# Optimization experiments

Measured on AMD Instinct MI355X. Metric: run time of the kernel, lower is better.

## Reference

```python
import jax, jax.numpy as jnp
import numpy as np

N_NODES = 50000

def _sage_conv(x, src, dst, W_l, b_l, W_r):
    # PyG SAGEConv, aggr='mean': out = lin_l(mean_j x_j) + lin_r(x_i)
    msg = x[src]                                                 # [E, d] gather
    agg = jax.ops.segment_sum(msg, dst, num_segments=N_NODES)   # [N, d] scatter-add
    cnt = jax.ops.segment_sum(jnp.ones((src.shape[0], 1), x.dtype), dst,
                              num_segments=N_NODES)              # [N, 1] in-degree
    agg = agg / jnp.maximum(cnt, 1.0)                            # mean (0 for isolated nodes)
    return agg @ W_l + b_l + x @ W_r

def setup_inputs() -> dict:
    key = jax.random.key(0)
    ks = jax.random.split(key, 8)
    in_f, hid, out_f = 128, 128, 64
    E = 640000
    x = jax.random.normal(ks[0], (N_NODES, in_f), dtype=jnp.float32)
    edge_index = jax.random.randint(ks[1], (2, E), 0, N_NODES, dtype=jnp.int64)
    def glorot(k, fan_in, fan_out):
        lim = (6.0 / (fan_in + fan_out)) ** 0.5
        return jax.random.uniform(k, (fan_in, fan_out), jnp.float32, -lim, lim)
    return {
        "x": x,
        "edge_index": edge_index,
        "W1_l": glorot(ks[2], in_f, hid),
        "b1": jnp.zeros((hid,), jnp.float32),
        "W1_r": glorot(ks[3], in_f, hid),
        "W2_l": glorot(ks[4], hid, out_f),
        "b2": jnp.zeros((out_f,), jnp.float32),
        "W2_r": glorot(ks[5], hid, out_f),
    }

def reference(x, edge_index, W1_l, b1, W1_r, W2_l, b2, W2_r):
    src, dst = edge_index[0], edge_index[1]
    h = _sage_conv(x, src, dst, W1_l, b1, W1_r)
    h = jax.nn.relu(h)
    # dropout: eval mode -> identity (deterministic reference)
    h = _sage_conv(h, src, dst, W2_l, b2, W2_r)
    return h
```

## Files before the change

### kernel.cpp

```cpp
#include <hip/hip_runtime.h>
#include <cstddef>

static constexpr int N_NODES = 50000;
static constexpr int E_EDGES = 640000;
static constexpr int F = 128;
static constexpr int MAXD = 64;
static constexpr int DEGS = 16;

typedef __bf16 b8 __attribute__((ext_vector_type(8)));
typedef float  f4 __attribute__((ext_vector_type(4)));
typedef float  f2 __attribute__((ext_vector_type(2)));

__device__ inline unsigned short f2bf(float f) {
    unsigned u = __float_as_uint(f);
    u += 0x7FFF + ((u >> 16) & 1);
    return (unsigned short)(u >> 16);
}

__device__ inline void accq(float* s, uint2 u) {
    f2 p;
    p = __builtin_amdgcn_cvt_pk_f32_fp8(u.x, false); s[0] += p.x; s[1] += p.y;
    p = __builtin_amdgcn_cvt_pk_f32_fp8(u.x, true);  s[2] += p.x; s[3] += p.y;
    p = __builtin_amdgcn_cvt_pk_f32_fp8(u.y, false); s[4] += p.x; s[5] += p.y;
    p = __builtin_amdgcn_cvt_pk_f32_fp8(u.y, true);  s[6] += p.x; s[7] += p.y;
}

template<int BN>
__device__ inline void pack_w_body(int t, const float* __restrict__ Wl,
                                   const float* __restrict__ Wr, uint4* __restrict__ Bp) {
    constexpr int NTg = BN / 16;
    int wid = t >> 6, lane = t & 63;
    if (wid >= 8 * NTg) return;
    int kq = lane >> 4, m = lane & 15;
    int kt = wid / NTg, nt = wid % NTg;
    unsigned short tmp[8];
#pragma unroll
    for (int j = 0; j < 8; ++j) {
        int k = kt * 32 + kq * 8 + j;
        const float* W = (k < 128) ? Wl : Wr;
        tmp[j] = f2bf(W[(size_t)(k & 127) * BN + nt * 16 + m]);
    }
    uint4 u;
    u.x = tmp[0] | ((unsigned)tmp[1] << 16);
    u.y = tmp[2] | ((unsigned)tmp[3] << 16);
    u.z = tmp[4] | ((unsigned)tmp[5] << 16);
    u.w = tmp[6] | ((unsigned)tmp[7] << 16);
    Bp[wid * 64 + lane] = u;
}

__global__ __launch_bounds__(256)
void prep(const int* __restrict__ ei, int* __restrict__ deg, int* __restrict__ col,
          const float* __restrict__ x, uint4* __restrict__ xb, uint2* __restrict__ xq,
          const float* __restrict__ W1l, const float* __restrict__ W1r, uint4* __restrict__ Bp1,
          const float* __restrict__ W2l, const float* __restrict__ W2r, uint4* __restrict__ Bp2) {
    int b = blockIdx.x, tid = threadIdx.x;
    if (b < 1250 && (b & 1) == 0) {
        int e0 = (b >> 1) * 1024 + tid;
        int s[4], d[4], r[4];
#pragma unroll
        for (int i = 0; i < 4; ++i) {
            s[i] = ei[e0 + i * 256];
            d[i] = ei[E_EDGES + e0 + i * 256];
        }
#pragma unroll
        for (int i = 0; i < 4; ++i)
            r[i] = atomicAdd(&deg[d[i] * DEGS], 1);
#pragma unroll
        for (int i = 0; i < 4; ++i)
            if (r[i] < MAXD) col[(d[i] << 6) + r[i]] = s[i];
    } else {
        int o = (b < 1250) ? (b >> 1) : (625 + (b - 1250));
        if (o < 3125) {
            int i = o * 256 + tid;
            const float4* s = (const float4*)x + (size_t)i * 2;
            float4 v0 = s[0], v1 = s[1];
            uint4 u;
            u.x = f2bf(v0.x) | ((unsigned)f2bf(v0.y) << 16);
            u.y = f2bf(v0.z) | ((unsigned)f2bf(v0.w) << 16);
            u.z = f2bf(v1.x) | ((unsigned)f2bf(v1.y) << 16);
            u.w = f2bf(v1.z) | ((unsigned)f2bf(v1.w) << 16);
            xb[i] = u;
            uint2 q;
            q.x = __builtin_amdgcn_cvt_pk_fp8_f32(v0.x, v0.y, 0, false);
            q.x = __builtin_amdgcn_cvt_pk_fp8_f32(v0.z, v0.w, q.x, true);
            q.y = __builtin_amdgcn_cvt_pk_fp8_f32(v1.x, v1.y, 0, false);
            q.y = __builtin_amdgcn_cvt_pk_fp8_f32(v1.z, v1.w, q.y, true);
            xq[i] = q;
        } else if (o < 3141) {
            pack_w_body<128>((o - 3125) * 256 + tid, W1l, W1r, Bp1);
        } else {
            pack_w_body<64>((o - 3141) * 256 + tid, W2l, W2r, Bp2);
        }
    }
}

__global__ __launch_bounds__(256)
void sage_l1(const uint2* __restrict__ featq,
             const unsigned short* __restrict__ featb,
             const int* __restrict__ deg,
             const int* __restrict__ col,
             const unsigned short* __restrict__ Bp1,
             const unsigned short* __restrict__ Bp2,
             const float* __restrict__ b1,
             const float* __restrict__ b2,
             unsigned char* __restrict__ Zq,
             float* __restrict__ out) {
    constexpr int LDW = 68;
    __shared__ unsigned Alds[16 * LDW];
    __shared__ unsigned short Hlds[16 * 136];

    const int tid  = threadIdx.x;
    const int wv   = tid >> 6;
    const int lane = tid & 63;
    const int c    = lane & 15;
    const int g    = lane >> 4;
    const int node0 = blockIdx.x * 16;
    const int node  = node0 + wv * 4 + g;

    {
        int d0 = deg[node * DEGS];
        int d  = d0 < MAXD ? d0 : MAXD;
        int jb = node << 6, je = jb + d;
        float s0[8] = {0.f,0.f,0.f,0.f,0.f,0.f,0.f,0.f};
        float s1[8] = {0.f,0.f,0.f,0.f,0.f,0.f,0.f,0.f};
        float s2[8] = {0.f,0.f,0.f,0.f,0.f,0.f,0.f,0.f};
        float s3[8] = {0.f,0.f,0.f,0.f,0.f,0.f,0.f,0.f};
        int j = jb;
        for (; j + 7 < je; j += 8) {
            uint2 u0 = featq[(size_t)col[j + 0] * 16 + c];
            uint2 u1 = featq[(size_t)col[j + 1] * 16 + c];
            uint2 u2 = featq[(size_t)col[j + 2] * 16 + c];
            uint2 u3 = featq[(size_t)col[j + 3] * 16 + c];
            uint2 u4 = featq[(size_t)col[j + 4] * 16 + c];
            uint2 u5 = featq[(size_t)col[j + 5] * 16 + c];
            uint2 u6 = featq[(size_t)col[j + 6] * 16 + c];
            uint2 u7 = featq[(size_t)col[j + 7] * 16 + c];
            accq(s0, u0); accq(s1, u1); accq(s2, u2); accq(s3, u3);
            accq(s0, u4); accq(s1, u5); accq(s2, u6); accq(s3, u7);
        }
        if (j + 3 < je) {
            uint2 u0 = featq[(size_t)col[j + 0] * 16 + c];
            uint2 u1 = featq[(size_t)col[j + 1] * 16 + c];
            uint2 u2 = featq[(size_t)col[j + 2] * 16 + c];
            uint2 u3 = featq[(size_t)col[j + 3] * 16 + c];
            accq(s0, u0); accq(s1, u1); accq(s2, u2); accq(s3, u3);
            j += 4;
        }
        for (; j < je; ++j) {
            uint2 u0 = featq[(size_t)col[j] * 16 + c];
            accq(s0, u0);
        }
        float inv = 1.0f / (float)(d > 0 ? d : 1);
        float r[8];
#pragma unroll
        for (int k = 0; k < 8; ++k) r[k] = ((s0[k] + s1[k]) + (s2[k] + s3[k])) * inv;
        uint4 o;
        o.x = f2bf(r[0]) | ((unsigned)f2bf(r[1]) << 16);
        o.y = f2bf(r[2]) | ((unsigned)f2bf(r[3]) << 16);
        o.z = f2bf(r[4]) | ((unsigned)f2bf(r[5]) << 16);
        o.w = f2bf(r[6]) | ((unsigned)f2bf(r[7]) << 16);
        *((uint4*)&Alds[(wv * 4 + g) * LDW + c * 4]) = o;
    }
    __syncthreads();

    const int m  = lane & 15;
    const int kq = lane >> 4;
    const unsigned short* srow = featb + (size_t)(node0 + m) * F + kq * 8;

    f4 zero = {0.f, 0.f, 0.f, 0.f};
    f4 acc[2] = {zero, zero};
#pragma unroll
    for (int kt = 0; kt < 8; ++kt) {
        b8 a;
        if (kt < 4) a = *((const b8*)((const char*)Alds + m * 272 + kt * 64 + kq * 16));
        else        a = *((const b8*)(srow + (kt - 4) * 32));
#pragma unroll
        for (int t = 0; t < 2; ++t) {
            int nt = wv * 2 + t;
            b8 b = *((const b8*)(Bp1 + ((size_t)(kt * 8 + nt) * 64 + lane) * 8));
            acc[t] = __builtin_amdgcn_mfma_f32_16x16x32_bf16(a, b, acc[t], 0, 0, 0);
        }
    }
    {
        int rowb = kq * 4;
#pragma unroll
        for (int t = 0; t < 2; ++t) {
            int cc = (wv * 2 + t) * 16 + m;
            float bv = b1[cc];
#pragma unroll
            for (int r = 0; r < 4; ++r) {
                float v = fmaxf(acc[t][r] + bv, 0.0f);
                Hlds[(rowb + r) * 136 + cc] = f2bf(v);
            }
        }
    }
    __syncthreads();

    f4 accZ = zero, accS = zero;
#pragma unroll
    for (int kt = 0; kt < 4; ++kt) {
        b8 a = *((const b8*)((const char*)Hlds + m * 272 + kt * 64 + kq * 16));
        b8 bz = *((const b8*)(Bp2 + ((size_t)(kt * 4 + wv) * 64 + lane) * 8));
        b8 bs = *((const b8*)(Bp2 + ((size_t)((kt + 4) * 4 + wv) * 64 + lane) * 8));
        accZ = __builtin_amdgcn_mfma_f32_16x16x32_bf16(a, bz, accZ, 0, 0, 0);
        accS = __builtin_amdgcn_mfma_f32_16x16x32_bf16(a, bs, accS, 0, 0, 0);
    }
    {
        int rowg = node0 + kq * 4;
        int cc = wv * 16 + m;
        float bv = b2[cc];
#pragma unroll
        for (int r = 0; r < 4; ++r) {
            unsigned q = __builtin_amdgcn_cvt_pk_fp8_f32(accZ[r], accZ[r], 0, false);
            Zq[(size_t)(rowg + r) * 64 + cc] = (unsigned char)(q & 0xFF);
            out[(size_t)(rowg + r) * 64 + cc] = accS[r] + bv;
        }
    }
}

__global__ __launch_bounds__(256)
void gather_add(const uint2* __restrict__ Zq,
                const int* __restrict__ deg,
                const int* __restrict__ col,
                float* __restrict__ out, int N) {
    int t = blockIdx.x * 256 + threadIdx.x;
    int node = t >> 3;
    if (node >= N) return;
    int c = t & 7;

    int d0 = deg[node * DEGS];
    int d  = d0 < MAXD ? d0 : MAXD;
    int jb = node << 6, je = jb + d;
    float s0[8] = {0.f,0.f,0.f,0.f,0.f,0.f,0.f,0.f};
    float s1[8] = {0.f,0.f,0.f,0.f,0.f,0.f,0.f,0.f};
    float s2[8] = {0.f,0.f,0.f,0.f,0.f,0.f,0.f,0.f};
    float s3[8] = {0.f,0.f,0.f,0.f,0.f,0.f,0.f,0.f};
    int j = jb;
    for (; j + 7 < je; j += 8) {
        uint2 u0 = Zq[(size_t)col[j + 0] * 8 + c];
        uint2 u1 = Zq[(size_t)col[j + 1] * 8 + c];
        uint2 u2 = Zq[(size_t)col[j + 2] * 8 + c];
        uint2 u3 = Zq[(size_t)col[j + 3] * 8 + c];
        uint2 u4 = Zq[(size_t)col[j + 4] * 8 + c];
        uint2 u5 = Zq[(size_t)col[j + 5] * 8 + c];
        uint2 u6 = Zq[(size_t)col[j + 6] * 8 + c];
        uint2 u7 = Zq[(size_t)col[j + 7] * 8 + c];
        accq(s0, u0); accq(s1, u1); accq(s2, u2); accq(s3, u3);
        accq(s0, u4); accq(s1, u5); accq(s2, u6); accq(s3, u7);
    }
    if (j + 3 < je) {
        uint2 u0 = Zq[(size_t)col[j + 0] * 8 + c];
        uint2 u1 = Zq[(size_t)col[j + 1] * 8 + c];
        uint2 u2 = Zq[(size_t)col[j + 2] * 8 + c];
        uint2 u3 = Zq[(size_t)col[j + 3] * 8 + c];
        accq(s0, u0); accq(s1, u1); accq(s2, u2); accq(s3, u3);
        j += 4;
    }
    for (; j < je; ++j) {
        uint2 u0 = Zq[(size_t)col[j] * 8 + c];
        accq(s0, u0);
    }
    float inv = 1.0f / (float)(d > 0 ? d : 1);
    float* op = out + (size_t)node * 64 + c * 8;
#pragma unroll
    for (int q = 0; q < 2; ++q) {
        float4 o = *((float4*)(op + q * 4));
        o.x += ((s0[q*4+0] + s1[q*4+0]) + (s2[q*4+0] + s3[q*4+0])) * inv;
        o.y += ((s0[q*4+1] + s1[q*4+1]) + (s2[q*4+1] + s3[q*4+1])) * inv;
        o.z += ((s0[q*4+2] + s1[q*4+2]) + (s2[q*4+2] + s3[q*4+2])) * inv;
        o.w += ((s0[q*4+3] + s1[q*4+3]) + (s2[q*4+3] + s3[q*4+3])) * inv;
        *((float4*)(op + q * 4)) = o;
    }
}


extern "C" void kernel_launch(void* const* d_in, const int* in_sizes, int n_in,
                              void* d_out, int out_size, void* d_ws, size_t ws_size,
                              hipStream_t stream) {
    const float* x   = (const float*)d_in[0];
    const int*   ei  = (const int*)d_in[1];
    const float* W1l = (const float*)d_in[2];
    const float* b1  = (const float*)d_in[3];
    const float* W1r = (const float*)d_in[4];
    const float* W2l = (const float*)d_in[5];
    const float* b2  = (const float*)d_in[6];
    const float* W2r = (const float*)d_in[7];
    float* out = (float*)d_out;

    unsigned* Zq    = (unsigned*)d_ws;
    unsigned* xb    = Zq + (size_t)N_NODES * 16;
    unsigned* xq    = xb + (size_t)N_NODES * 64;
    unsigned* Bp1   = xq + (size_t)N_NODES * 32;
    unsigned* Bp2   = Bp1 + 16384;
    int* col        = (int*)(Bp2 + 8192);
    int* deg        = col + (size_t)N_NODES * MAXD;

    hipMemsetAsync(deg, 0, (size_t)N_NODES * DEGS * sizeof(int), stream);

    prep<<<3774, 256, 0, stream>>>(ei, deg, col, x, (uint4*)xb, (uint2*)xq,
                                   W1l, W1r, (uint4*)Bp1, W2l, W2r, (uint4*)Bp2);

    sage_l1<<<N_NODES / 16, 256, 0, stream>>>(
        (const uint2*)xq, (const unsigned short*)xb, deg, col,
        (const unsigned short*)Bp1, (const unsigned short*)Bp2,
        b1, b2, (unsigned char*)Zq, out);

    gather_add<<<(N_NODES * 8 + 255) / 256, 256, 0, stream>>>(
        (const uint2*)Zq, deg, col, out, N_NODES);
}
```

Baseline: 172.3 us.

## Replace global atomic CSR build with two-pass binned bucketing through shared memory

Edge-to-CSR construction no longer does one global atomicAdd per edge on a padded degree array. Edges are first binned by destination block (256 nodes per bin) using shared-memory counters and one global atomic per bin per block, then a new bucket kernel builds per-node column lists with LDS atomics and writes a compact deg array. This cuts contended global atomics and the large degree memset, at the cost of an extra kernel launch and an intermediate bin buffer. Packing source indices into 16 bits assumes node ids below 65536, and bins are capped at 4096 entries.

```diff
diff --git a/kernel.cpp b/kernel.cpp
--- a/kernel.cpp
+++ b/kernel.cpp
@@ -5,7 +5,9 @@
 static constexpr int E_EDGES = 640000;
 static constexpr int F = 128;
 static constexpr int MAXD = 64;
-static constexpr int DEGS = 16;
+static constexpr int NBINS = 196;
+static constexpr int BINCAP = 4096;
+static constexpr int EBLK  = 250;
 
 typedef __bf16 b8 __attribute__((ext_vector_type(8)));
 typedef float  f4 __attribute__((ext_vector_type(4)));
@@ -49,27 +51,37 @@
 }
 
 __global__ __launch_bounds__(256)
-void prep(const int* __restrict__ ei, int* __restrict__ deg, int* __restrict__ col,
+void prep(const int* __restrict__ ei, int* __restrict__ gbin, unsigned* __restrict__ binbuf,
           const float* __restrict__ x, uint4* __restrict__ xb, uint2* __restrict__ xq,
           const float* __restrict__ W1l, const float* __restrict__ W1r, uint4* __restrict__ Bp1,
           const float* __restrict__ W2l, const float* __restrict__ W2r, uint4* __restrict__ Bp2) {
     int b = blockIdx.x, tid = threadIdx.x;
-    if (b < 1250 && (b & 1) == 0) {
-        int e0 = (b >> 1) * 1024 + tid;
-        int s[4], d[4], r[4];
-#pragma unroll
-        for (int i = 0; i < 4; ++i) {
-            s[i] = ei[e0 + i * 256];
-            d[i] = ei[E_EDGES + e0 + i * 256];
-        }
-#pragma unroll
-        for (int i = 0; i < 4; ++i)
-            r[i] = atomicAdd(&deg[d[i] * DEGS], 1);
-#pragma unroll
-        for (int i = 0; i < 4; ++i)
-            if (r[i] < MAXD) col[(d[i] << 6) + r[i]] = s[i];
+    if (b < EBLK) {
+        __shared__ int cnt[NBINS];
+        __shared__ int base[NBINS];
+        for (int i = tid; i < NBINS; i += 256) cnt[i] = 0;
+        __syncthreads();
+        int e0 = b * 2560;
+        unsigned rec[10]; int bin[10]; int rnk[10];
+#pragma unroll
+        for (int k = 0; k < 10; ++k) {
+            int e = e0 + k * 256 + tid;
+            int s = ei[e], d = ei[E_EDGES + e];
+            bin[k] = d >> 8;
+            rec[k] = ((unsigned)(d & 255) << 16) | (unsigned)s;
+            rnk[k] = atomicAdd(&cnt[bin[k]], 1);
+        }
+        __syncthreads();
+        for (int i = tid; i < NBINS; i += 256)
+            base[i] = atomicAdd(&gbin[i], cnt[i]);
+        __syncthreads();
+#pragma unroll
+        for (int k = 0; k < 10; ++k) {
+            int pos = base[bin[k]] + rnk[k];
+            if (pos < BINCAP) binbuf[(size_t)bin[k] * BINCAP + pos] = rec[k];
+        }
     } else {
-        int o = (b < 1250) ? (b >> 1) : (625 + (b - 1250));
+        int o = b - EBLK;
         if (o < 3125) {
             int i = o * 256 + tid;
             const float4* s = (const float4*)x + (size_t)i * 2;
@@ -95,6 +107,27 @@
 }
 
 __global__ __launch_bounds__(256)
+void bucket(const unsigned* __restrict__ binbuf, const int* __restrict__ gbin,
+            int* __restrict__ deg, int* __restrict__ col) {
+    int b = blockIdx.x, tid = threadIdx.x;
+    __shared__ int lc[256];
+    lc[tid] = 0;
+    __syncthreads();
+    int cnt = gbin[b]; cnt = cnt < BINCAP ? cnt : BINCAP;
+    const unsigned* bb = binbuf + (size_t)b * BINCAP;
+    for (int i = tid; i < cnt; i += 256) {
+        unsigned rec = bb[i];
+        int dl = (rec >> 16) & 255;
+        int s  = (int)(rec & 0xFFFFu);
+        int r  = atomicAdd(&lc[dl], 1);
+        if (r < MAXD) col[(((size_t)(b << 8) + dl) << 6) + r] = s;
+    }
+    __syncthreads();
+    int node = (b << 8) + tid;
+    if (node < N_NODES) deg[node] = lc[tid];
+}
+
+__global__ __launch_bounds__(256)
 void sage_l1(const uint2* __restrict__ featq,
              const unsigned short* __restrict__ featb,
              const int* __restrict__ deg,
@@ -118,7 +151,7 @@
     const int node  = node0 + wv * 4 + g;
 
     {
-        int d0 = deg[node * DEGS];
+        int d0 = deg[node];
         int d  = d0 < MAXD ? d0 : MAXD;
         int jb = node << 6, je = jb + d;
         float s0[8] = {0.f,0.f,0.f,0.f,0.f,0.f,0.f,0.f};
@@ -228,7 +261,7 @@
     if (node >= N) return;
     int c = t & 7;
 
-    int d0 = deg[node * DEGS];
+    int d0 = deg[node];
     int d  = d0 < MAXD ? d0 : MAXD;
     int jb = node << 6, je = jb + d;
     float s0[8] = {0.f,0.f,0.f,0.f,0.f,0.f,0.f,0.f};
@@ -294,11 +327,15 @@
     unsigned* Bp2   = Bp1 + 16384;
     int* col        = (int*)(Bp2 + 8192);
     int* deg        = col + (size_t)N_NODES * MAXD;
-
-    hipMemsetAsync(deg, 0, (size_t)N_NODES * DEGS * sizeof(int), stream);
-
-    prep<<<3774, 256, 0, stream>>>(ei, deg, col, x, (uint4*)xb, (uint2*)xq,
-                                   W1l, W1r, (uint4*)Bp1, W2l, W2r, (uint4*)Bp2);
+    int* gbin       = deg + N_NODES;
+    unsigned* binbuf = (unsigned*)(gbin + 256);
+
+    hipMemsetAsync(gbin, 0, 256 * sizeof(int), stream);
+
+    prep<<<EBLK + 3149, 256, 0, stream>>>(ei, gbin, binbuf, x, (uint4*)xb, (uint2*)xq,
+                                          W1l, W1r, (uint4*)Bp1, W2l, W2r, (uint4*)Bp2);
+
+    bucket<<<NBINS, 256, 0, stream>>>(binbuf, gbin, deg, col);
 
     sage_l1<<<N_NODES / 16, 256, 0, stream>>>(
         (const uint2*)xq, (const unsigned short*)xb, deg, col,
```

Result: faster. 156.1 us (-9.4%).
